# Performance work log

Hardware: AMD Instinct MI355X
Metric: run time of the kernel (lower is better)

The kernel has to match this reference:

```python
import jax, jax.numpy as jnp
import numpy as np

B, NA, NE = 1024, 15, 16
N_AGENTS = NA + 1
BN = B * N_AGENTS
D_OWN = D_ALL = D_EN = 32
H, NH, NMOVE, RD = 256, 4, 6, 8
HD = H // NH
GATE = 1.0
NEG = -1e9  # stand-in for -inf (safe under autodiff)


def _gelu(x):
    return jax.nn.gelu(x, approximate=False)  # torch nn.GELU default is exact


def _ln(x, g, b, eps=1e-5):
    m = x.mean(-1, keepdims=True)
    v = ((x - m) ** 2).mean(-1, keepdims=True)
    return (x - m) * jax.lax.rsqrt(v + eps) * g + b


def _masked_mean(x, mask, axis):
    w = mask[..., None].astype(x.dtype)
    return (x * w).sum(axis) / jnp.clip(w.sum(axis), 1e-8)


def _mha(q, kv, mask, Wq, Wk, Wv, Wo):
    # q: [BN,H], kv: [BN,M,H], mask: [BN,M] bool
    bn = q.shape[0]
    qh = (q @ Wq.T).reshape(bn, NH, HD)
    kh = (kv @ Wk.T).reshape(bn, -1, NH, HD)
    vh = (kv @ Wv.T).reshape(bn, -1, NH, HD)
    scores = jnp.einsum('bhd,bmhd->bhm', qh, kh) / np.sqrt(HD)
    scores = jnp.where(mask[:, None, :], scores, NEG)
    attn = jax.nn.softmax(scores, axis=-1)
    ctx = jnp.einsum('bhm,bmhd->bhd', attn, vh).reshape(bn, H)
    return ctx @ Wo.T


def setup_inputs() -> dict:
    key = jax.random.key(0)
    ks = iter(jax.random.split(key, 64))
    nrm = lambda *s: jax.random.normal(next(ks), s, dtype=jnp.float32)
    w = lambda o, i: nrm(o, i) * 0.02
    inp = dict(
        bs=B,
        own_feats=nrm(BN, 1, D_OWN),
        ally_feats=nrm(BN, NA, D_ALL),
        enemy_feats=nrm(BN, NE, D_EN),
        hidden_state=nrm(B, N_AGENTS, H),
        own_W=w(H, D_OWN), own_b=jnp.zeros(H),
        ally_W=w(H, D_ALL), ally_b=jnp.zeros(H),
        en_W=w(H, D_EN), en_b=jnp.zeros(H),
        aA_Wq=w(H, H), aA_Wk=w(H, H), aA_Wv=w(H, H), aA_Wo=w(H, H),
        aE_Wq=w(H, H), aE_Wk=w(H, H), aE_Wv=w(H, H), aE_Wo=w(H, H),
        fuse_W1=w(H, 3 * H), fuse_b1=jnp.zeros(H), fuse_g1=jnp.ones(H), fuse_be1=jnp.zeros(H),
        fuse_W2=w(H, H), fuse_b2=jnp.zeros(H),
        pool_W1=w(128, 3 * H), pool_b1=jnp.zeros(128), pool_g1=jnp.ones(128), pool_be1=jnp.zeros(128),
        pool_W2=w(128, 128), pool_b2=jnp.zeros(128),
        role_W1=w(128, 128), role_b1=jnp.zeros(128), role_g1=jnp.ones(128), role_be1=jnp.zeros(128),
        role_W2=w(RD, 128), role_b2=jnp.zeros(RD),
        rln_g=jnp.ones(RD), rln_b=jnp.zeros(RD),
        gru_Wih=w(3 * H, H + RD), gru_Whh=w(3 * H, H),
        gru_bih=jnp.zeros(3 * H), gru_bhh=jnp.zeros(3 * H),
        qn_W=w(NMOVE, H), qn_b=jnp.zeros(NMOVE),
        qp_W=w(H, H + RD), kp_W=w(H, H),
    )
    return inp


def reference(bs, own_feats, ally_feats, enemy_feats, hidden_state,
              own_W, own_b, ally_W, ally_b, en_W, en_b,
              aA_Wq, aA_Wk, aA_Wv, aA_Wo, aE_Wq, aE_Wk, aE_Wv, aE_Wo,
              fuse_W1, fuse_b1, fuse_g1, fuse_be1, fuse_W2, fuse_b2,
              pool_W1, pool_b1, pool_g1, pool_be1, pool_W2, pool_b2,
              role_W1, role_b1, role_g1, role_be1, role_W2, role_b2,
              rln_g, rln_b, gru_Wih, gru_Whh, gru_bih, gru_bhh,
              qn_W, qn_b, qp_W, kp_W):
    ally_mask = ~jnp.all(ally_feats == 0, axis=-1)   # [BN,Na]
    enemy_mask = ~jnp.all(enemy_feats == 0, axis=-1)  # [BN,Ne]

    own_e = own_feats @ own_W.T + own_b        # [BN,1,H]
    ally_e = ally_feats @ ally_W.T + ally_b    # [BN,Na,H]
    enemy_e = enemy_feats @ en_W.T + en_b      # [BN,Ne,H]
    self_emb = own_e[:, 0]                     # [BN,H]

    cA = _mha(self_emb, ally_e, ally_mask, aA_Wq, aA_Wk, aA_Wv, aA_Wo)
    cE = _mha(self_emb, enemy_e, enemy_mask, aE_Wq, aE_Wk, aE_Wv, aE_Wo)

    # fuse MLP: Linear -> GELU -> LN -> Linear
    f_in = jnp.concatenate([self_emb, cA, cE], axis=-1)
    h0 = _ln(_gelu(f_in @ fuse_W1.T + fuse_b1), fuse_g1, fuse_be1) @ fuse_W2.T + fuse_b2

    pA = _masked_mean(ally_e, ally_mask, 1)
    pE = _masked_mean(enemy_e, enemy_mask, 1)
    p_in = jnp.concatenate([self_emb, pA, pE], axis=-1)
    pooled = _ln(_gelu(p_in @ pool_W1.T + pool_b1), pool_g1, pool_be1) @ pool_W2.T + pool_b2
    r = jnp.tanh(_ln(_gelu(pooled @ role_W1.T + role_b1), role_g1, role_be1) @ role_W2.T + role_b2)
    r = _ln(r, rln_g, rln_b)

    # GRUCell (torch convention)
    h_prev = hidden_state.reshape(-1, H)
    x = jnp.concatenate([h0, GATE * r], axis=-1)
    gi = x @ gru_Wih.T + gru_bih
    gh = h_prev @ gru_Whh.T + gru_bhh
    i_r, i_z, i_n = jnp.split(gi, 3, axis=-1)
    h_r, h_z, h_n = jnp.split(gh, 3, axis=-1)
    rg = jax.nn.sigmoid(i_r + h_r)
    zg = jax.nn.sigmoid(i_z + h_z)
    ng = jnp.tanh(i_n + rg * h_n)
    h_cur = (1.0 - zg) * ng + zg * h_prev

    q_normal = h_cur @ qn_W.T + qn_b  # [BN,n_move]

    q_vec = jnp.concatenate([h_cur, GATE * r], axis=-1) @ qp_W.T  # [BN,H]
    k_vec = enemy_e @ kp_W.T                                       # [BN,Ne,H]
    logits = jnp.einsum('bj,bmj->bm', q_vec, k_vec) / np.sqrt(H)
    logits = jnp.where(enemy_mask, logits, NEG)
    denom = jnp.clip(enemy_mask.sum(-1, keepdims=True), 1).astype(logits.dtype)
    mean_valid = jnp.where(enemy_mask, logits, 0.0).sum(-1, keepdims=True) / denom
    q_interact = logits - mean_valid

    Q = jnp.concatenate([q_normal, q_interact], axis=-1)
    h_out = h_cur.reshape(bs, N_AGENTS, H)
    return Q, h_out
```

## Files before the change

### kernel.cpp

```cpp
#include <hip/hip_runtime.h>
#include <hip/hip_bf16.h>


#define MROWS 16384

typedef __attribute__((ext_vector_type(8))) short short8;
typedef __attribute__((ext_vector_type(4))) float float4v;

__device__ __forceinline__ unsigned short f2b(float f) {
    __hip_bfloat16 h = __float2bfloat16(f);
    return *reinterpret_cast<unsigned short*>(&h);
}
__device__ __forceinline__ float b2f(unsigned short u) {
    __hip_bfloat16 h;
    *reinterpret_cast<unsigned short*>(&h) = u;
    return __bfloat162float(h);
}
__device__ __forceinline__ void gll16(const unsigned short* g, unsigned short* l) {
    __builtin_amdgcn_global_load_lds((const __attribute__((address_space(1))) void*)g,
                                     (__attribute__((address_space(3))) void*)l, 16, 0, 0);
}

__global__ void cvt_misc(const float* __restrict__ hidden, const float* __restrict__ ownf,
                         unsigned short* __restrict__ XG, unsigned short* __restrict__ OWNb,
// ... 1 lines not shown
    int idx = blockIdx.x * 256 + threadIdx.x;
    const int nh = MROWS * 64;
    const int no = MROWS * 8;
    if (idx < nh) {
        int row = idx >> 6, c4 = (idx & 63) * 4;
        float4 v = *(const float4*)(hidden + (size_t)row * 256 + c4);
        unsigned short* d = XG + (size_t)row * 520 + 264 + c4;
        d[0] = f2b(v.x); d[1] = f2b(v.y); d[2] = f2b(v.z); d[3] = f2b(v.w);
    } else if (idx < nh + no) {
        int j = idx - nh;
        int row = j >> 3, c4 = (j & 7) * 4;
        float4 v = *(const float4*)(ownf + (size_t)row * 32 + c4);
        unsigned short* d = OWNb + (size_t)row * 32 + c4;
        d[0] = f2b(v.x); d[1] = f2b(v.y); d[2] = f2b(v.z); d[3] = f2b(v.w);
    } else if (idx < nh + no + 16) {
        int j = idx - nh - no;
        ((uint4*)zbuf)[j] = make_uint4(0u, 0u, 0u, 0u);
    }
}

struct TOp {
    int type;
    const float* A; int sAi, sAk;
    const float* B; int sBj, sBk;
    void* O; int sOi;
    int I, J, K;
    int nb; int aB, bB, oB;
};
struct TOpSet { int n; int tiles[26]; TOp ops[26]; };

__global__ __launch_bounds__(256)
void compose_tiled(TOpSet S) {
    int t = blockIdx.x;
    int op = 0;
    while (op < S.n && t >= S.tiles[op]) { t -= S.tiles[op]; op++; }
    if (op >= S.n) return;
    TOp o = S.ops[op];
    int ti = (o.I + 31) >> 5, tj = (o.J + 31) >> 5;
    int per = ti * tj;
    int b = t / per;
    int rem = t - b * per;
    int i0 = (rem / tj) * 32, j0 = (rem % tj) * 32;
    int tid = threadIdx.x;
    if (o.type >= 2) {
        for (int e = tid; e < 1024; e += 256) {
            int r = e >> 5, c = e & 31;
            int i = i0 + r, j = j0 + c;
            if (i < o.I && j < o.J) {
                unsigned short v = 0;
                if (o.type == 2) v = f2b(o.A[(long)b * o.aB + (long)i * o.sAi + (long)j * o.sAk]);
                ((unsigned short*)o.O)[(long)b * o.oB + (long)i * o.sOi + j] = v;
            }
        }
        return;
    }
    __shared__ float As[32][33];
    __shared__ float Bs[32][33];
    int tx = tid & 15, ty = tid >> 4;
    float a00 = 0.f, a01 = 0.f, a10 = 0.f, a11 = 0.f;
    const float* Ab = o.A + (long)b * o.aB;
    const float* Bb = o.B + (long)b * o.bB;
    for (int k0 = 0; k0 < o.K; k0 += 32) {
        for (int e = tid; e < 1024; e += 256) {
            int r = e >> 5, c = e & 31;
            As[r][c] = (i0 + r < o.I && k0 + c < o.K)
                       ? Ab[(long)(i0 + r) * o.sAi + (long)(k0 + c) * o.sAk] : 0.f;
// ... 5 lines not shown
        for (int k = 0; k < 32; k++) {
            float x0 = As[ty * 2][k], x1 = As[ty * 2 + 1][k];
            float y0 = Bs[k][tx * 2], y1 = Bs[k][tx * 2 + 1];
            a00 += x0 * y0; a01 += x0 * y1; a10 += x1 * y0; a11 += x1 * y1;
        }
        __syncthreads();
    }
    int i = i0 + ty * 2, j = j0 + tx * 2;
    float vals[2][2] = {{a00, a01}, {a10, a11}};
#pragma unroll
    for (int di = 0; di < 2; di++)
#pragma unroll
        for (int dj = 0; dj < 2; dj++) {
            int ii = i + di, jj = j + dj;
            if (ii < o.I && jj < o.J) {
                long oidx = (long)b * o.oB + (long)ii * o.sOi + jj;
                if (o.type == 0) ((unsigned short*)o.O)[oidx] = f2b(vals[di][dj]);
                else ((float*)o.O)[oidx] = vals[di][dj];
            }
        }
}

struct MOp { const float* A; int sAi; const float* x; const float* b1; const float* b2; float* out; int I, K; };
struct MOpSet { int n; int waves[10]; MOp ops[10]; };

__global__ void mv_ops(MOpSet S) {
    int wid = blockIdx.x * 4 + (threadIdx.x >> 6);
    int lane = threadIdx.x & 63;
    int op = 0;
    while (op < S.n && wid >= S.waves[op]) { wid -= S.waves[op]; op++; }
    if (op >= S.n) return;
    MOp o = S.ops[op];
    float s = 0.f;
    for (int k = lane; k < o.K; k += 64) s += o.A[(long)wid * o.sAi + k] * o.x[k];
    for (int off = 32; off; off >>= 1) s += __shfl_xor(s, off, 64);
    if (lane == 0) {
        if (o.b1) s += o.b1[wid];
        if (o.b2) s += o.b2[wid];
        o.out[wid] = s;
    }
}

__global__ __launch_bounds__(256, 4)
void gemm_bf16(const unsigned short* __restrict__ A, int lda,
               const unsigned short* __restrict__ W,
               const float* __restrict__ bias,
               unsigned short* __restrict__ C, int ldc,
               int N, int K, int act,
               const unsigned short* __restrict__ zbuf) {
    __shared__ __align__(16) unsigned short As[128 * 32];
    __shared__ __align__(16) unsigned short Bs[128 * 32];
    int tid = threadIdx.x;
    int m0 = blockIdx.x * 128, n0 = blockIdx.y * 128;
    int wave = tid >> 6, lane = tid & 63;
    int wm = (wave & 1) * 64, wn = (wave >> 1) * 64;
    int l16 = lane & 15, quad = lane >> 4;

    float4v acc[4][4];
#pragma unroll
    for (int i = 0; i < 4; i++)
#pragma unroll
        for (int j = 0; j < 4; j++) acc[i][j] = (float4v){0.f, 0.f, 0.f, 0.f};

    int s0 = tid, s1 = tid + 256;
    int row0 = s0 >> 2, seg0 = (s0 & 3) * 8;
    int row1 = s1 >> 2, seg1 = (s1 & 3) * 8;
    const unsigned short* Arow0 = A + (size_t)(m0 + row0) * lda;
    const unsigned short* Arow1 = A + (size_t)(m0 + row1) * lda;
    const unsigned short* Wrow0 = (n0 + row0 < N) ? W + (size_t)(n0 + row0) * K : nullptr;
    const unsigned short* Wrow1 = (n0 + row1 < N) ? W + (size_t)(n0 + row1) * K : nullptr;
    unsigned short* ldsA0 = As + (size_t)(wave * 64) * 8;
    unsigned short* ldsA1 = As + (size_t)(wave * 64 + 256) * 8;
    unsigned short* ldsB0 = Bs + (size_t)(wave * 64) * 8;
    unsigned short* ldsB1 = Bs + (size_t)(wave * 64 + 256) * 8;

    for (int k0 = 0; k0 < K; k0 += 32) {
        int ka0 = k0 + seg0, ka1 = k0 + seg1;
        gll16((ka0 < K) ? Arow0 + ka0 : zbuf, ldsA0);
        gll16((ka1 < K) ? Arow1 + ka1 : zbuf, ldsA1);
        gll16((ka0 < K && Wrow0) ? Wrow0 + ka0 : zbuf, ldsB0);
        gll16((ka1 < K && Wrow1) ? Wrow1 + ka1 : zbuf, ldsB1);
        __syncthreads();
        short8 a[4], b[4];
#pragma unroll
        for (int i = 0; i < 4; i++) {
            a[i] = *(const short8*)(&As[(wm + i * 16 + l16) * 32 + quad * 8]);
            b[i] = *(const short8*)(&Bs[(wn + i * 16 + l16) * 32 + quad * 8]);
        }
#pragma unroll
        for (int i = 0; i < 4; i++)
#pragma unroll
            for (int j = 0; j < 4; j++)
                acc[i][j] = __builtin_amdgcn_mfma_f32_16x16x32_bf16(a[i], b[j], acc[i][j], 0, 0, 0);
        __syncthreads();
    }
#pragma unroll
    for (int i = 0; i < 4; i++) {
#pragma unroll
        for (int j = 0; j < 4; j++) {
#pragma unroll
            for (int rr = 0; rr < 4; rr++) {
                int rowm = m0 + wm + i * 16 + quad * 4 + rr;
                int coln = wn + j * 16 + l16;
                if (n0 + coln >= N) continue;
                float v = acc[i][j][rr];
                if (bias) v += bias[n0 + coln];
                if (act == 1) v = 0.5f * v * (1.f + erff(v * 0.70710678f));
                C[(size_t)rowm * ldc + n0 + coln] = f2b(v);
            }
        }
    }
}

__global__ void ln_fp(const unsigned short* __restrict__ FPC,
                      const float* __restrict__ g1, const float* __restrict__ be1,
                      const float* __restrict__ g2, const float* __restrict__ be2,
                      unsigned short* __restrict__ XG, unsigned short* __restrict__ T2) {
    int row = blockIdx.x, t = threadIdx.x;
    float v = b2f(FPC[(size_t)row * 384 + t]);
// ... 7 lines not shown
        float ts = rs[0] + rs[1] + rs[2] + rs[3], tq = rq[0] + rq[1] + rq[2] + rq[3];
        float mean = ts * (1.f / 256.f);
        float var = tq * (1.f / 256.f) - mean * mean;
        float o = (v - mean) * rsqrtf(var + 1e-5f) * g1[t] + be1[t];
        XG[(size_t)row * 520 + t] = f2b(o);
    } else {
        int tt = t - 256;
        float ts = rs[4] + rs[5], tq = rq[4] + rq[5];
        float mean = ts * (1.f / 128.f);
        float var = tq * (1.f / 128.f) - mean * mean;
        float o = (v - mean) * rsqrtf(var + 1e-5f) * g2[tt] + be2[tt];
        T2[(size_t)row * 128 + tt] = f2b(o);
    }
}

__global__ __launch_bounds__(256)
void glue_attn(const float* __restrict__ allyf, const float* __restrict__ enemyf,
               const float* __restrict__ ownf, const unsigned short* __restrict__ QKS,
               unsigned short* __restrict__ X) {
    __shared__ float af[4][495];
    __shared__ float ef[4][528];
    __shared__ float qk[4][256];
    __shared__ float attnA[4][64];
    __shared__ float attnE[4][64];
    __shared__ float mskA[4][16];
    __shared__ float mskE[4][16];
    int tid = threadIdx.x;
    size_t rb = (size_t)blockIdx.x * 4;

    for (int idx = tid; idx < 1920; idx += 256) {
        int r = idx / 480, w0 = idx % 480;
        af[r][(w0 >> 5) * 33 + (w0 & 31)] = allyf[(rb + r) * 480 + w0];
    }
    for (int idx = tid; idx < 2048; idx += 256) {
        int r = idx >> 9, w0 = idx & 511;
        ef[r][(w0 >> 5) * 33 + (w0 & 31)] = enemyf[(rb + r) * 512 + w0];
    }
    for (int idx = tid; idx < 1024; idx += 256)
        qk[idx >> 8][idx & 255] = b2f(QKS[(rb + (idx >> 8)) * 256 + (idx & 255)]);
    if (tid < 128) {
        int r = tid >> 5, c = tid & 31;
        X[(rb + r) * 360 + c] = f2b(ownf[(rb + r) * 32 + c]);
    } else if (tid < 152) {
        int r = (tid - 128) / 6, c = 98 + (tid - 128) % 6;
        X[(rb + r) * 360 + c] = 0;
    }
    __syncthreads();

    {
        int r = tid >> 6, lane = tid & 63;
        if (lane < 15) {
            bool nz = false;
            for (int d = 0; d < 32; d++) nz |= (af[r][lane * 33 + d] != 0.f);
            mskA[r][lane] = nz ? 1.f : 0.f;
        } else if (lane == 15) {
            mskA[r][15] = 0.f;
        } else if (lane < 32) {
            int mm = lane - 16;
            bool nz = false;
            for (int d = 0; d < 32; d++) nz |= (ef[r][mm * 33 + d] != 0.f);
            mskE[r][mm] = nz ? 1.f : 0.f;
        }
    }
    __syncthreads();

    int r = tid >> 6, lane = tid & 63;
    int h = lane >> 4, m = lane & 15;
    {
        float sc = -3.0e38f;
        if (m < 15) {
            float s = 0.f;
            for (int d = 0; d < 32; d++) s += qk[r][h * 32 + d] * af[r][m * 33 + d];
            sc = (mskA[r][m] > 0.f) ? s * 0.125f : -1e9f;
        }
        float mx = sc;
        for (int o = 8; o; o >>= 1) mx = fmaxf(mx, __shfl_xor(mx, o, 64));
        float e = (m < 15) ? __expf(sc - mx) : 0.f;
        float sm = e;
        for (int o = 8; o; o >>= 1) sm += __shfl_xor(sm, o, 64);
        attnA[r][h * 16 + m] = e / sm;
    }
// ... 62 lines not shown
    float acc = b2[t];
    const float* w = W2 + t * 128;
    for (int d = 0; d < 128; d++)
        acc += w[d] * ((t3[r][d] - mean) * rstd * gl[d] + bl[d]);
    float v = tanhf(acc);
    float mn = v;
    for (int o = 4; o; o >>= 1) mn += __shfl_xor(mn, o, 8);
    mn *= 0.125f;
    float dv = v - mn, qq = dv * dv;
    for (int o = 4; o; o >>= 1) qq += __shfl_xor(qq, o, 8);
    qq *= 0.125f;
    size_t row = (size_t)blockIdx.x * 32 + r;
    XG[row * 520 + 256 + t] = f2b(dv * rsqrtf(qq + 1e-5f) * rg[t] + rb[t]);
}

__global__ void glue_gru(const unsigned short* __restrict__ G, const float* __restrict__ hp,
                         float* __restrict__ hout, unsigned short* __restrict__ XQ,
                         const unsigned short* __restrict__ XG) {
    size_t row = blockIdx.x;
    int i = threadIdx.x;
    size_t b = row * 1024;
    float rg = 1.f / (1.f + __expf(-b2f(G[b + i])));
    float zg = 1.f / (1.f + __expf(-b2f(G[b + 256 + i])));
    float ng = tanhf(b2f(G[b + 512 + i]) + rg * b2f(G[b + 768 + i]));
    float h = (1.f - zg) * ng + zg * hp[row * 256 + i];
    hout[row * 256 + i] = h;
    XQ[row * 264 + i] = f2b(h);
    if (i < 8) XQ[row * 264 + 256 + i] = XG[row * 520 + 256 + i];
}

__global__ __launch_bounds__(256)
void glue_final(const unsigned short* __restrict__ QWS, const float* __restrict__ efeats,
                const float* __restrict__ qnb, float* __restrict__ Q) {
    __shared__ float ef[8][528];
    __shared__ float qw[8][40];
    int tid = threadIdx.x;
    size_t rb = (size_t)blockIdx.x * 8;
    for (int idx = tid; idx < 4096; idx += 256) {
        int r = idx >> 9, w0 = idx & 511;
        ef[r][(w0 >> 5) * 33 + (w0 & 31)] = efeats[(rb + r) * 512 + w0];
    }
    for (int idx = tid; idx < 320; idx += 256) {
        int r = idx / 40, c = idx % 40;
        qw[r][c] = b2f(QWS[(rb + r) * 40 + c]);
    }
    __syncthreads();
    int r = tid >> 5, t = tid & 31;
    size_t row = rb + r;
    float lg = 0.f, mk = 0.f;
    if (t < 16) {
        const float* fr = ef[r] + t * 33;
        bool nz = false;
        float s = 0.f;
        for (int d = 0; d < 32; d++) { nz |= (fr[d] != 0.f); s += qw[r][d] * fr[d]; }
        mk = nz ? 1.f : 0.f;
        lg = (s + qw[r][32]) * 0.0625f;
    }
    float sv = mk * lg, cv = mk;
    for (int o = 8; o; o >>= 1) { sv += __shfl_xor(sv, o, 64); cv += __shfl_xor(cv, o, 64); }
    float mean = sv / fmaxf(cv, 1.f);
    if (t < 16) Q[row * 22 + 6 + t] = (mk > 0.f ? lg : -1e9f) - mean;
    if (t < 6) Q[row * 22 + t] = qw[r][33 + t] + qnb[t];
}

extern "C" void kernel_launch(void* const* d_in, const int* in_sizes, int n_in,
                              void* d_out, int out_size, void* d_ws, size_t ws_size,
                              hipStream_t stream) {
    const float* own_feats = (const float*)d_in[1];
    const float* ally_feats = (const float*)d_in[2];
    const float* enemy_feats = (const float*)d_in[3];
    const float* hidden = (const float*)d_in[4];
    const float* own_W = (const float*)d_in[5];   const float* own_b = (const float*)d_in[6];
    const float* ally_W = (const float*)d_in[7];  const float* ally_b = (const float*)d_in[8];
    const float* en_W = (const float*)d_in[9];    const float* en_b = (const float*)d_in[10];
    const float* aA_Wq = (const float*)d_in[11];  const float* aA_Wk = (const float*)d_in[12];
    const float* aA_Wv = (const float*)d_in[13];  const float* aA_Wo = (const float*)d_in[14];
    const float* aE_Wq = (const float*)d_in[15];  const float* aE_Wk = (const float*)d_in[16];
// ... 9 lines not shown
    const float* role_W2 = (const float*)d_in[35]; const float* role_b2 = (const float*)d_in[36];
    const float* rln_g = (const float*)d_in[37];   const float* rln_b = (const float*)d_in[38];
    const float* gru_Wih = (const float*)d_in[39]; const float* gru_Whh = (const float*)d_in[40];
    const float* gru_bih = (const float*)d_in[41]; const float* gru_bhh = (const float*)d_in[42];
    const float* qn_W = (const float*)d_in[43];    const float* qn_b = (const float*)d_in[44];
    const float* qp_W = (const float*)d_in[45];    const float* kp_W = (const float*)d_in[46];

    char* wsp = (char*)d_ws;
    size_t off = 0;
    auto alloc = [&](size_t bytes) { void* p = wsp + off; off = (off + bytes + 255) & ~(size_t)255; return p; };

    unsigned short* X    = (unsigned short*)alloc((size_t)MROWS * 360 * 2);
    unsigned short* XG   = (unsigned short*)alloc((size_t)MROWS * 520 * 2);
    unsigned short* FPC  = (unsigned short*)alloc((size_t)MROWS * 384 * 2);
    unsigned short* GIb  = (unsigned short*)alloc((size_t)MROWS * 1024 * 2);
    unsigned short* XQ   = (unsigned short*)alloc((size_t)MROWS * 264 * 2);
    unsigned short* T2b  = (unsigned short*)alloc((size_t)MROWS * 128 * 2);
    unsigned short* T3b  = (unsigned short*)alloc((size_t)MROWS * 128 * 2);
    unsigned short* QKSb = (unsigned short*)alloc((size_t)MROWS * 256 * 2);
    unsigned short* QWSb = (unsigned short*)alloc((size_t)MROWS * 40 * 2);
    unsigned short* OWNb = (unsigned short*)alloc((size_t)MROWS * 32 * 2);
    unsigned short* FPW  = (unsigned short*)alloc(384 * 360 * 2);
    unsigned short* WGRU = (unsigned short*)alloc(1024 * 520 * 2);
    unsigned short* QWSW = (unsigned short*)alloc(40 * 264 * 2);
    unsigned short* WQKSO= (unsigned short*)alloc(256 * 32 * 2);
    unsigned short* rpW  = (unsigned short*)alloc(128 * 128 * 2);
    unsigned short* zbuf = (unsigned short*)alloc(256);
    float* WkAp = (float*)alloc(256 * 32 * 4);
    float* WvAp = (float*)alloc(256 * 32 * 4);
    float* WkEp = (float*)alloc(256 * 32 * 4);
    float* WvEp = (float*)alloc(256 * 32 * 4);
    float* Wkpp = (float*)alloc(256 * 32 * 4);
    float* WQKS_AE = (float*)alloc(256 * 256 * 4);
    float* WoVA = (float*)alloc(256 * 128 * 4);
    float* WoVE = (float*)alloc(256 * 128 * 4);
    float* bvAp = (float*)alloc(256 * 4);
    float* bvEp = (float*)alloc(256 * 4);
    float* bkpp = (float*)alloc(256 * 4);
    float* vall = (float*)alloc(768 * 4);
    float* qksb = (float*)alloc(256 * 4);
    float* fpb  = (float*)alloc(384 * 4);
    float* gbias= (float*)alloc(1024 * 4);
    float* rpb  = (float*)alloc(128 * 4);

    float* Qout = (float*)d_out;
    float* Hout = Qout + (size_t)MROWS * 22;

    auto tilesOf = [](const TOp& o) {
        return o.nb * (((o.I + 31) / 32) * ((o.J + 31) / 32));
    };

    cvt_misc<<<(MROWS * 64 + MROWS * 8 + 16 + 255) / 256, 256, 0, stream>>>(hidden, own_feats, XG, OWNb, zbuf);

    {
        MOpSet S; S.n = 5; int waves = 0;
        S.ops[0] = {aA_Wv, 256, ally_b, nullptr, nullptr, bvAp, 256, 256};
        S.ops[1] = {aE_Wv, 256, en_b, nullptr, nullptr, bvEp, 256, 256};
        S.ops[2] = {kp_W, 256, en_b, nullptr, nullptr, bkpp, 256, 256};
        S.ops[3] = {nullptr, 0, nullptr, own_b, nullptr, vall, 256, 0};
        S.ops[4] = {role_W1, 128, pool_b2, role_b1, nullptr, rpb, 128, 128};
        for (int i = 0; i < S.n; i++) { S.waves[i] = S.ops[i].I; waves += S.ops[i].I; }
        mv_ops<<<(waves + 3) / 4, 256, 0, stream>>>(S);
    }
    {
        TOpSet S; S.n = 0; int grid = 0;
        auto add = [&](TOp o) { S.tiles[S.n] = tilesOf(o); grid += S.tiles[S.n]; S.ops[S.n++] = o; };
        add({1, aA_Wk, 256, 1, ally_W, 1, 32, WkAp, 32, 256, 32, 256, 1, 0, 0, 0});
        add({1, aA_Wv, 256, 1, ally_W, 1, 32, WvAp, 32, 256, 32, 256, 1, 0, 0, 0});
        add({1, aE_Wk, 256, 1, en_W, 1, 32, WkEp, 32, 256, 32, 256, 1, 0, 0, 0});
        add({1, aE_Wv, 256, 1, en_W, 1, 32, WvEp, 32, 256, 32, 256, 1, 0, 0, 0});
        add({1, kp_W, 256, 1, en_W, 1, 32, Wkpp, 32, 256, 32, 256, 1, 0, 0, 0});
        compose_tiled<<<grid, 256, 0, stream>>>(S);
    }
    {
        TOpSet S; S.n = 0; int grid = 0;
        auto add = [&](TOp o) { S.tiles[S.n] = tilesOf(o); grid += S.tiles[S.n]; S.ops[S.n++] = o; };
        add({1, WkAp, 1, 32, aA_Wq, 1, 256, WQKS_AE, 256, 32, 256, 64, 4, 2048, 16384, 8192});
        add({1, WkEp, 1, 32, aE_Wq, 1, 256, WQKS_AE + 128 * 256, 256, 32, 256, 64, 4, 2048, 16384, 8192});
        add({1, aA_Wo, 256, 1, WvAp, 1, 32, WoVA, 128, 256, 32, 64, 4, 64, 2048, 32});
        add({1, aE_Wo, 256, 1, WvEp, 1, 32, WoVE, 128, 256, 32, 64, 4, 64, 2048, 32});
        compose_tiled<<<grid, 256, 0, stream>>>(S);
    }
    {
        MOpSet S; S.n = 3; int waves = 0;
        S.ops[0] = {aA_Wo, 256, bvAp, nullptr, nullptr, vall + 256, 256, 256};
        S.ops[1] = {aE_Wo, 256, bvEp, nullptr, nullptr, vall + 512, 256, 256};
        S.ops[2] = {WQKS_AE, 256, own_b, nullptr, nullptr, qksb, 256, 256};
        for (int i = 0; i < S.n; i++) { S.waves[i] = S.ops[i].I; waves += S.ops[i].I; }
        mv_ops<<<(waves + 3) / 4, 256, 0, stream>>>(S);
    }
    {
        MOpSet S; S.n = 5; int waves = 0;
        S.ops[0] = {fuse_W1, 768, vall, fuse_b1, nullptr, fpb, 256, 768};
        S.ops[1] = {pool_W1, 768, vall, pool_b1, nullptr, fpb + 256, 128, 256};
        S.ops[2] = {gru_Wih, 264, fuse_b2, gru_bih, gru_bhh, gbias, 512, 256};
        S.ops[3] = {gru_Wih + 512 * 264, 264, fuse_b2, gru_bih + 512, nullptr, gbias + 512, 256, 256};
        S.ops[4] = {nullptr, 0, nullptr, gru_bhh + 512, nullptr, gbias + 768, 256, 0};
        for (int i = 0; i < S.n; i++) { S.waves[i] = S.ops[i].I; waves += S.ops[i].I; }
        mv_ops<<<(waves + 3) / 4, 256, 0, stream>>>(S);
    }
    {
        TOpSet S; S.n = 0; int grid = 0;
        auto add = [&](TOp o) { S.tiles[S.n] = tilesOf(o); grid += S.tiles[S.n]; S.ops[S.n++] = o; };
        add({0, fuse_W1, 768, 1, own_W, 1, 32, FPW, 360, 256, 32, 256, 1, 0, 0, 0});
        add({3, nullptr, 0, 0, nullptr, 0, 0, FPW + 32, 360, 256, 72, 0, 1, 0, 0, 0});
        add({0, fuse_W1 + 256, 768, 1, WoVA, 1, 128, FPW + 104, 360, 256, 128, 256, 1, 0, 0, 0});
        add({0, fuse_W1 + 512, 768, 1, WoVE, 1, 128, FPW + 232, 360, 256, 128, 256, 1, 0, 0, 0});
        add({0, pool_W1, 768, 1, own_W, 1, 32, FPW + 256 * 360, 360, 128, 32, 256, 1, 0, 0, 0});
        add({0, pool_W1 + 256, 768, 1, ally_W, 1, 32, FPW + 256 * 360 + 32, 360, 128, 32, 256, 1, 0, 0, 0});
        add({0, pool_W1 + 512, 768, 1, en_W, 1, 32, FPW + 256 * 360 + 64, 360, 128, 32, 256, 1, 0, 0, 0});
        add({0, pool_W1 + 256, 768, 1, ally_b, 0, 1, FPW + 256 * 360 + 96, 360, 128, 1, 256, 1, 0, 0, 0});
        add({0, pool_W1 + 512, 768, 1, en_b, 0, 1, FPW + 256 * 360 + 97, 360, 128, 1, 256, 1, 0, 0, 0});
        add({3, nullptr, 0, 0, nullptr, 0, 0, FPW + 256 * 360 + 98, 360, 128, 262, 0, 1, 0, 0, 0});
        add({0, gru_Wih, 264, 1, fuse_W2, 1, 256, WGRU, 520, 512, 256, 256, 1, 0, 0, 0});
        add({2, gru_Wih + 256, 264, 1, nullptr, 0, 0, WGRU + 256, 520, 512, 8, 0, 1, 0, 0, 0});
        add({2, gru_Whh, 256, 1, nullptr, 0, 0, WGRU + 264, 520, 512, 256, 0, 1, 0, 0, 0});
        add({0, gru_Wih + 512 * 264, 264, 1, fuse_W2, 1, 256, WGRU + 512 * 520, 520, 256, 256, 256, 1, 0, 0, 0});
        add({2, gru_Wih + 512 * 264 + 256, 264, 1, nullptr, 0, 0, WGRU + 512 * 520 + 256, 520, 256, 8, 0, 1, 0, 0, 0});
        add({3, nullptr, 0, 0, nullptr, 0, 0, WGRU + 512 * 520 + 264, 520, 256, 256, 0, 1, 0, 0, 0});
        add({3, nullptr, 0, 0, nullptr, 0, 0, WGRU + 768 * 520, 520, 256, 264, 0, 1, 0, 0, 0});
        add({2, gru_Whh + 512 * 256, 256, 1, nullptr, 0, 0, WGRU + 768 * 520 + 264, 520, 256, 256, 0, 1, 0, 0, 0});
        add({0, Wkpp, 1, 32, qp_W, 1, 264, QWSW, 264, 32, 264, 256, 1, 0, 0, 0});
        add({0, bkpp, 0, 1, qp_W, 1, 264, QWSW + 32 * 264, 264, 1, 264, 256, 1, 0, 0, 0});
        add({2, qn_W, 256, 1, nullptr, 0, 0, QWSW + 33 * 264, 264, 6, 256, 0, 1, 0, 0, 0});
        add({3, nullptr, 0, 0, nullptr, 0, 0, QWSW + 33 * 264 + 256, 264, 6, 8, 0, 1, 0, 0, 0});
        add({3, nullptr, 0, 0, nullptr, 0, 0, QWSW + 39 * 264, 264, 1, 264, 0, 1, 0, 0, 0});
        add({0, WQKS_AE, 256, 1, own_W, 1, 32, WQKSO, 32, 256, 32, 256, 1, 0, 0, 0});
        add({0, role_W1, 128, 1, pool_W2, 1, 128, rpW, 128, 128, 128, 128, 1, 0, 0, 0});
        compose_tiled<<<grid, 256, 0, stream>>>(S);
    }

    auto gemm = [&](const unsigned short* A, int lda, const unsigned short* Wm, const float* bias,
                    unsigned short* C, int ldc, int N, int K, int act) {
        gemm_bf16<<<dim3(MROWS / 128, (N + 127) / 128), 256, 0, stream>>>(A, lda, Wm, bias, C, ldc, N, K, act, zbuf);
    };

    gemm(OWNb, 32, WQKSO, qksb, QKSb, 256, 256, 32, 0);
    glue_attn<<<MROWS / 4, 256, 0, stream>>>(ally_feats, enemy_feats, own_feats, QKSb, X);
    gemm(X, 360, FPW, fpb, FPC, 384, 384, 360, 1);
    ln_fp<<<MROWS, 384, 0, stream>>>(FPC, fuse_g1, fuse_be1, pool_g1, pool_be1, XG, T2b);
    gemm(T2b, 128, rpW, rpb, T3b, 128, 128, 128, 1);
    ln_role<<<MROWS / 32, 256, 0, stream>>>(T3b, role_g1, role_be1, role_W2, role_b2, rln_g, rln_b, XG);
    gemm(XG, 520, WGRU, gbias, GIb, 1024, 1024, 520, 0);
    glue_gru<<<MROWS, 256, 0, stream>>>(GIb, hidden, Hout, XQ, XG);
    gemm(XQ, 264, QWSW, nullptr, QWSb, 40, 40, 264, 0);
    glue_final<<<MROWS / 8, 256, 0, stream>>>(QWSb, enemy_feats, qn_b, Qout);
}
```

Baseline: 485.9 us.

## Split GRU GEMM to skip zero blocks, fuse GRU tail with Q head, merge prep launches

```diff
diff --git a/kernel.cpp b/kernel.cpp
--- a/kernel.cpp
+++ b/kernel.cpp
@@ -39,8 +39,7 @@
         unsigned short* d = OWNb + (size_t)row * 32 + c4;
         d[0] = f2b(v.x); d[1] = f2b(v.y); d[2] = f2b(v.z); d[3] = f2b(v.w);
     } else if (idx < nh + no + 16) {
-        int j = idx - nh - no;
-        ((uint4*)zbuf)[j] = make_uint4(0u, 0u, 0u, 0u);
+        ((uint4*)zbuf)[idx - nh - no] = make_uint4(0u, 0u, 0u, 0u);
     }
 }
 
@@ -51,6 +50,7 @@
     void* O; int sOi;
     int I, J, K;
     int nb; int aB, bB, oB;
+    const float* bias1; const float* bias2;
 };
 struct TOpSet { int n; int tiles[26]; TOp ops[26]; };
 
@@ -72,9 +72,13 @@
             int r = e >> 5, c = e & 31;
             int i = i0 + r, j = j0 + c;
             if (i < o.I && j < o.J) {
-                unsigned short v = 0;
-                if (o.type == 2) v = f2b(o.A[(long)b * o.aB + (long)i * o.sAi + (long)j * o.sAk]);
-                ((unsigned short*)o.O)[(long)b * o.oB + (long)i * o.sOi + j] = v;
+                long oidx = (long)b * o.oB + (long)i * o.sOi + j;
+                if (o.type == 3) { ((unsigned short*)o.O)[oidx] = 0; }
+                else {
+                    float v = o.A[(long)b * o.aB + (long)i * o.sAi + (long)j * o.sAk];
+                    if (o.type == 2) ((unsigned short*)o.O)[oidx] = f2b(v);
+                    else ((float*)o.O)[oidx] = v;
+                }
             }
         }
         return;
@@ -110,31 +114,14 @@
         for (int dj = 0; dj < 2; dj++) {
             int ii = i + di, jj = j + dj;
             if (ii < o.I && jj < o.J) {
+                float v = vals[di][dj];
+                if (o.bias1) v += o.bias1[ii];
+                if (o.bias2) v += o.bias2[ii];
                 long oidx = (long)b * o.oB + (long)ii * o.sOi + jj;
-                if (o.type == 0) ((unsigned short*)o.O)[oidx] = f2b(vals[di][dj]);
-                else ((float*)o.O)[oidx] = vals[di][dj];
+                if (o.type == 0) ((unsigned short*)o.O)[oidx] = f2b(v);
+                else ((float*)o.O)[oidx] = v;
             }
         }
-}
-
-struct MOp { const float* A; int sAi; const float* x; const float* b1; const float* b2; float* out; int I, K; };
-struct MOpSet { int n; int waves[10]; MOp ops[10]; };
-
-__global__ void mv_ops(MOpSet S) {
-    int wid = blockIdx.x * 4 + (threadIdx.x >> 6);
-    int lane = threadIdx.x & 63;
-    int op = 0;
-    while (op < S.n && wid >= S.waves[op]) { wid -= S.waves[op]; op++; }
-    if (op >= S.n) return;
-    MOp o = S.ops[op];
-    float s = 0.f;
-    for (int k = lane; k < o.K; k += 64) s += o.A[(long)wid * o.sAi + k] * o.x[k];
-    for (int off = 32; off; off >>= 1) s += __shfl_xor(s, off, 64);
-    if (lane == 0) {
-        if (o.b1) s += o.b1[wid];
-        if (o.b2) s += o.b2[wid];
-        o.out[wid] = s;
-    }
 }
 
 __global__ __launch_bounds__(256, 4)
@@ -147,7 +134,7 @@
     __shared__ __align__(16) unsigned short As[128 * 32];
     __shared__ __align__(16) unsigned short Bs[128 * 32];
     int tid = threadIdx.x;
-    int m0 = blockIdx.x * 128, n0 = blockIdx.y * 128;
+    int n0 = blockIdx.x * 128, m0 = blockIdx.y * 128;
     int wave = tid >> 6, lane = tid & 63;
     int wm = (wave & 1) * 64, wn = (wave >> 1) * 64;
     int l16 = lane & 15, quad = lane >> 4;
@@ -163,8 +150,8 @@
     int row1 = s1 >> 2, seg1 = (s1 & 3) * 8;
     const unsigned short* Arow0 = A + (size_t)(m0 + row0) * lda;
     const unsigned short* Arow1 = A + (size_t)(m0 + row1) * lda;
-    const unsigned short* Wrow0 = (n0 + row0 < N) ? W + (size_t)(n0 + row0) * K : nullptr;
-    const unsigned short* Wrow1 = (n0 + row1 < N) ? W + (size_t)(n0 + row1) * K : nullptr;
+    const unsigned short* Wrow0 = W + (size_t)(n0 + row0) * K;
+    const unsigned short* Wrow1 = W + (size_t)(n0 + row1) * K;
     unsigned short* ldsA0 = As + (size_t)(wave * 64) * 8;
     unsigned short* ldsA1 = As + (size_t)(wave * 64 + 256) * 8;
     unsigned short* ldsB0 = Bs + (size_t)(wave * 64) * 8;
@@ -174,8 +161,8 @@
         int ka0 = k0 + seg0, ka1 = k0 + seg1;
         gll16((ka0 < K) ? Arow0 + ka0 : zbuf, ldsA0);
         gll16((ka1 < K) ? Arow1 + ka1 : zbuf, ldsA1);
-        gll16((ka0 < K && Wrow0) ? Wrow0 + ka0 : zbuf, ldsB0);
-        gll16((ka1 < K && Wrow1) ? Wrow1 + ka1 : zbuf, ldsB1);
+        gll16((ka0 < K) ? Wrow0 + ka0 : zbuf, ldsB0);
+        gll16((ka1 < K) ? Wrow1 + ka1 : zbuf, ldsB1);
         __syncthreads();
         short8 a[4], b[4];
 #pragma unroll
@@ -198,7 +185,6 @@
             for (int rr = 0; rr < 4; rr++) {
                 int rowm = m0 + wm + i * 16 + quad * 4 + rr;
                 int coln = wn + j * 16 + l16;
-                if (n0 + coln >= N) continue;
                 float v = acc[i][j][rr];
                 if (bias) v += bias[n0 + coln];
                 if (act == 1) v = 0.5f * v * (1.f + erff(v * 0.70710678f));
@@ -236,57 +222,58 @@
     }
 }
 
-__global__ __launch_bounds__(256)
+__global__ __launch_bounds__(128)
 void glue_attn(const float* __restrict__ allyf, const float* __restrict__ enemyf,
                const float* __restrict__ ownf, const unsigned short* __restrict__ QKS,
                unsigned short* __restrict__ X) {
-    __shared__ float af[4][495];
-    __shared__ float ef[4][528];
-    __shared__ float qk[4][256];
-    __shared__ float attnA[4][64];
-    __shared__ float attnE[4][64];
-    __shared__ float mskA[4][16];
-    __shared__ float mskE[4][16];
+    __shared__ float af[2][495];
+    __shared__ float ef[2][528];
+    __shared__ float qk[2][256];
+    __shared__ float attnA[2][64];
+    __shared__ float attnE[2][64];
+    __shared__ float mskA[2][16];
+    __shared__ float mskE[2][16];
     int tid = threadIdx.x;
-    size_t rb = (size_t)blockIdx.x * 4;
-
-    for (int idx = tid; idx < 1920; idx += 256) {
-        int r = idx / 480, w0 = idx % 480;
-        af[r][(w0 >> 5) * 33 + (w0 & 31)] = allyf[(rb + r) * 480 + w0];
-    }
-    for (int idx = tid; idx < 2048; idx += 256) {
-        int r = idx >> 9, w0 = idx & 511;
-        ef[r][(w0 >> 5) * 33 + (w0 & 31)] = enemyf[(rb + r) * 512 + w0];
-    }
-    for (int idx = tid; idx < 1024; idx += 256)
+    size_t rb = (size_t)blockIdx.x * 2;
+
+    for (int idx = tid; idx < 240; idx += 128) {
+        int r = idx / 120, w0 = (idx % 120) * 4;
+        float4 v = *(const float4*)(allyf + (rb + r) * 480 + w0);
+        float* d = &af[r][(w0 >> 5) * 33 + (w0 & 31)];
+        d[0] = v.x; d[1] = v.y; d[2] = v.z; d[3] = v.w;
+    }
+    for (int idx = tid; idx < 256; idx += 128) {
+        int r = idx >> 7, w0 = (idx & 127) * 4;
+        float4 v = *(const float4*)(enemyf + (rb + r) * 512 + w0);
+        float* d = &ef[r][(w0 >> 5) * 33 + (w0 & 31)];
+        d[0] = v.x; d[1] = v.y; d[2] = v.z; d[3] = v.w;
+    }
+    for (int idx = tid; idx < 512; idx += 128)
         qk[idx >> 8][idx & 255] = b2f(QKS[(rb + (idx >> 8)) * 256 + (idx & 255)]);
-    if (tid < 128) {
+    if (tid < 64) {
         int r = tid >> 5, c = tid & 31;
         X[(rb + r) * 360 + c] = f2b(ownf[(rb + r) * 32 + c]);
-    } else if (tid < 152) {
-        int r = (tid - 128) / 6, c = 98 + (tid - 128) % 6;
+    } else if (tid < 76) {
+        int j = tid - 64, r = j / 6, c = 98 + j % 6;
         X[(rb + r) * 360 + c] = 0;
     }
     __syncthreads();
 
-    {
-        int r = tid >> 6, lane = tid & 63;
-        if (lane < 15) {
-            bool nz = false;
-            for (int d = 0; d < 32; d++) nz |= (af[r][lane * 33 + d] != 0.f);
-            mskA[r][lane] = nz ? 1.f : 0.f;
-        } else if (lane == 15) {
-            mskA[r][15] = 0.f;
-        } else if (lane < 32) {
-            int mm = lane - 16;
-            bool nz = false;
-            for (int d = 0; d < 32; d++) nz |= (ef[r][mm * 33 + d] != 0.f);
-            mskE[r][mm] = nz ? 1.f : 0.f;
-        }
-    }
-    __syncthreads();
-
     int r = tid >> 6, lane = tid & 63;
+    if (lane < 15) {
+        bool nz = false;
+        for (int d = 0; d < 32; d++) nz |= (af[r][lane * 33 + d] != 0.f);
+        mskA[r][lane] = nz ? 1.f : 0.f;
+    } else if (lane == 15) {
+        mskA[r][15] = 0.f;
+    } else if (lane < 32) {
+        int mm = lane - 16;
+        bool nz = false;
+        for (int d = 0; d < 32; d++) nz |= (ef[r][mm * 33 + d] != 0.f);
+        mskE[r][mm] = nz ? 1.f : 0.f;
+    }
+    __syncthreads();
+
     int h = lane >> 4, m = lane & 15;
     {
         float sc = -3.0e38f;
@@ -379,53 +366,55 @@
     XG[row * 520 + 256 + t] = f2b(dv * rsqrtf(qq + 1e-5f) * rg[t] + rb[t]);
 }
 
-__global__ void glue_gru(const unsigned short* __restrict__ G, const float* __restrict__ hp,
-                         float* __restrict__ hout, unsigned short* __restrict__ XQ,
-                         const unsigned short* __restrict__ XG) {
+__global__ __launch_bounds__(320)
+void glue_tail(const unsigned short* __restrict__ G, const float* __restrict__ hp,
+               const unsigned short* __restrict__ XG, const unsigned short* __restrict__ QWSW,
+               const float* __restrict__ enemyf, const float* __restrict__ qnb,
+               float* __restrict__ Q, float* __restrict__ Hout) {
+    __shared__ float xq[264];
+    __shared__ float efs[528];
+    __shared__ float qws[40];
     size_t row = blockIdx.x;
-    int i = threadIdx.x;
-    size_t b = row * 1024;
-    float rg = 1.f / (1.f + __expf(-b2f(G[b + i])));
-    float zg = 1.f / (1.f + __expf(-b2f(G[b + 256 + i])));
-    float ng = tanhf(b2f(G[b + 512 + i]) + rg * b2f(G[b + 768 + i]));
-    float h = (1.f - zg) * ng + zg * hp[row * 256 + i];
-    hout[row * 256 + i] = h;
-    XQ[row * 264 + i] = f2b(h);
-    if (i < 8) XQ[row * 264 + 256 + i] = XG[row * 520 + 256 + i];
-}
-
-__global__ __launch_bounds__(256)
-void glue_final(const unsigned short* __restrict__ QWS, const float* __restrict__ efeats,
-                const float* __restrict__ qnb, float* __restrict__ Q) {
-    __shared__ float ef[8][528];
-    __shared__ float qw[8][40];
-    int tid = threadIdx.x;
-    size_t rb = (size_t)blockIdx.x * 8;
-    for (int idx = tid; idx < 4096; idx += 256) {
-        int r = idx >> 9, w0 = idx & 511;
-        ef[r][(w0 >> 5) * 33 + (w0 & 31)] = efeats[(rb + r) * 512 + w0];
-    }
-    for (int idx = tid; idx < 320; idx += 256) {
-        int r = idx / 40, c = idx % 40;
-        qw[r][c] = b2f(QWS[(rb + r) * 40 + c]);
-    }
-    __syncthreads();
-    int r = tid >> 5, t = tid & 31;
-    size_t row = rb + r;
-    float lg = 0.f, mk = 0.f;
+    int t = threadIdx.x;
+    for (int idx = t; idx < 512; idx += 320)
+        efs[(idx >> 5) * 33 + (idx & 31)] = enemyf[row * 512 + idx];
+    if (t < 256) {
+        size_t b = row * 1024;
+        float rg = 1.f / (1.f + __expf(-b2f(G[b + t])));
+        float zg = 1.f / (1.f + __expf(-b2f(G[b + 256 + t])));
+        float ng = tanhf(b2f(G[b + 512 + t]) + rg * b2f(G[b + 768 + t]));
+        float h = (1.f - zg) * ng + zg * hp[row * 256 + t];
+        Hout[row * 256 + t] = h;
+        xq[t] = h;
+    } else if (t < 264) {
+        xq[t] = b2f(XG[row * 520 + t]);
+    }
+    __syncthreads();
+    {
+        int o = t >> 3, sub = t & 7;
+        const unsigned short* wr = QWSW + o * 264 + sub * 33;
+        const float* xv = xq + sub * 33;
+        float s = 0.f;
+        for (int i = 0; i < 33; i++) s += b2f(wr[i]) * xv[i];
+        for (int off = 4; off; off >>= 1) s += __shfl_xor(s, off, 8);
+        if (sub == 0) qws[o] = s;
+    }
+    __syncthreads();
     if (t < 16) {
-        const float* fr = ef[r] + t * 33;
+        const float* fr = efs + t * 33;
         bool nz = false;
         float s = 0.f;
-        for (int d = 0; d < 32; d++) { nz |= (fr[d] != 0.f); s += qw[r][d] * fr[d]; }
-        mk = nz ? 1.f : 0.f;
-        lg = (s + qw[r][32]) * 0.0625f;
-    }
-    float sv = mk * lg, cv = mk;
-    for (int o = 8; o; o >>= 1) { sv += __shfl_xor(sv, o, 64); cv += __shfl_xor(cv, o, 64); }
-    float mean = sv / fmaxf(cv, 1.f);
-    if (t < 16) Q[row * 22 + 6 + t] = (mk > 0.f ? lg : -1e9f) - mean;
-    if (t < 6) Q[row * 22 + t] = qw[r][33 + t] + qnb[t];
+        for (int d = 0; d < 32; d++) { nz |= (fr[d] != 0.f); s += qws[d] * fr[d]; }
+        float mk = nz ? 1.f : 0.f;
+        float lg = (s + qws[32]) * 0.0625f;
+        float sv = mk * lg, cv = mk;
+        for (int o = 8; o; o >>= 1) { sv += __shfl_xor(sv, o, 16); cv += __shfl_xor(cv, o, 16); }
+        float mean = sv / fmaxf(cv, 1.f);
+        Q[row * 22 + 6 + t] = (mk > 0.f ? lg : -1e9f) - mean;
+    } else if (t >= 64 && t < 70) {
+        int j = t - 64;
+        Q[row * 22 + j] = qws[33 + j] + qnb[j];
+    }
 }
 
 extern "C" void kernel_launch(void* const* d_in, const int* in_sizes, int n_in,
@@ -465,14 +454,14 @@
     unsigned short* XG   = (unsigned short*)alloc((size_t)MROWS * 520 * 2);
     unsigned short* FPC  = (unsigned short*)alloc((size_t)MROWS * 384 * 2);
     unsigned short* GIb  = (unsigned short*)alloc((size_t)MROWS * 1024 * 2);
-    unsigned short* XQ   = (unsigned short*)alloc((size_t)MROWS * 264 * 2);
     unsigned short* T2b  = (unsigned short*)alloc((size_t)MROWS * 128 * 2);
     unsigned short* T3b  = (unsigned short*)alloc((size_t)MROWS * 128 * 2);
     unsigned short* QKSb = (unsigned short*)alloc((size_t)MROWS * 256 * 2);
-    unsigned short* QWSb = (unsigned short*)alloc((size_t)MROWS * 40 * 2);
     unsigned short* OWNb = (unsigned short*)alloc((size_t)MROWS * 32 * 2);
     unsigned short* FPW  = (unsigned short*)alloc(384 * 360 * 2);
-    unsigned short* WGRU = (unsigned short*)alloc(1024 * 520 * 2);
+    unsigned short* WRZ  = (unsigned short*)alloc(512 * 520 * 2);
+    unsigned short* WIN  = (unsigned short*)alloc(256 * 264 * 2);
+    unsigned short* WHN  = (unsigned short*)alloc(256 * 256 * 2);
     unsigned short* QWSW = (unsigned short*)alloc(40 * 264 * 2);
     unsigned short* WQKSO= (unsigned short*)alloc(256 * 32 * 2);
     unsigned short* rpW  = (unsigned short*)alloc(128 * 128 * 2);
@@ -497,6 +486,13 @@
     float* Qout = (float*)d_out;
     float* Hout = Qout + (size_t)MROWS * 22;
 
+    auto mk = [](int type, const float* A, int sAi, int sAk, const float* B, int sBj, int sBk,
+                 void* O, int sOi, int I, int J, int K, int nb = 1, int aB = 0, int bB = 0,
+                 int oB = 0, const float* b1 = nullptr, const float* b2 = nullptr) {
+        TOp o; o.type = type; o.A = A; o.sAi = sAi; o.sAk = sAk; o.B = B; o.sBj = sBj;
+        o.sBk = sBk; o.O = O; o.sOi = sOi; o.I = I; o.J = J; o.K = K; o.nb = nb;
+        o.aB = aB; o.bB = bB; o.oB = oB; o.bias1 = b1; o.bias2 = b2; return o;
+    };
     auto tilesOf = [](const TOp& o) {
         return o.nb * (((o.I + 31) / 32) * ((o.J + 31) / 32));
     };
@@ -504,96 +500,79 @@
     cvt_misc<<<(MROWS * 64 + MROWS * 8 + 16 + 255) / 256, 256, 0, stream>>>(hidden, own_feats, XG, OWNb, zbuf);
 
     {
-        MOpSet S; S.n = 5; int waves = 0;
-        S.ops[0] = {aA_Wv, 256, ally_b, nullptr, nullptr, bvAp, 256, 256};
-        S.ops[1] = {aE_Wv, 256, en_b, nullptr, nullptr, bvEp, 256, 256};
-        S.ops[2] = {kp_W, 256, en_b, nullptr, nullptr, bkpp, 256, 256};
-        S.ops[3] = {nullptr, 0, nullptr, own_b, nullptr, vall, 256, 0};
-        S.ops[4] = {role_W1, 128, pool_b2, role_b1, nullptr, rpb, 128, 128};
-        for (int i = 0; i < S.n; i++) { S.waves[i] = S.ops[i].I; waves += S.ops[i].I; }
-        mv_ops<<<(waves + 3) / 4, 256, 0, stream>>>(S);
+        TOpSet S; S.n = 0; int grid = 0;
+        auto add = [&](TOp o) { S.tiles[S.n] = tilesOf(o); grid += S.tiles[S.n]; S.ops[S.n++] = o; };
+        add(mk(1, aA_Wk, 256, 1, ally_W, 1, 32, WkAp, 32, 256, 32, 256));
+        add(mk(1, aA_Wv, 256, 1, ally_W, 1, 32, WvAp, 32, 256, 32, 256));
+        add(mk(1, aE_Wk, 256, 1, en_W, 1, 32, WkEp, 32, 256, 32, 256));
+        add(mk(1, aE_Wv, 256, 1, en_W, 1, 32, WvEp, 32, 256, 32, 256));
+        add(mk(1, kp_W, 256, 1, en_W, 1, 32, Wkpp, 32, 256, 32, 256));
+        add(mk(1, aA_Wv, 256, 1, ally_b, 0, 1, bvAp, 1, 256, 1, 256));
+        add(mk(1, aE_Wv, 256, 1, en_b, 0, 1, bvEp, 1, 256, 1, 256));
+        add(mk(1, kp_W, 256, 1, en_b, 0, 1, bkpp, 1, 256, 1, 256));
+        add(mk(4, own_b, 1, 1, nullptr, 0, 0, vall, 1, 256, 1, 0));
+        add(mk(1, role_W1, 128, 1, pool_b2, 0, 1, rpb, 1, 128, 1, 128, 1, 0, 0, 0, role_b1));
+        add(mk(1, gru_Wih, 264, 1, fuse_b2, 0, 1, gbias, 1, 512, 1, 256, 1, 0, 0, 0, gru_bih, gru_bhh));
+        add(mk(1, gru_Wih + 512 * 264, 264, 1, fuse_b2, 0, 1, gbias + 512, 1, 256, 1, 256, 1, 0, 0, 0, gru_bih + 512));
+        add(mk(4, gru_bhh + 512, 1, 1, nullptr, 0, 0, gbias + 768, 1, 256, 1, 0));
+        compose_tiled<<<grid, 256, 0, stream>>>(S);
     }
     {
         TOpSet S; S.n = 0; int grid = 0;
         auto add = [&](TOp o) { S.tiles[S.n] = tilesOf(o); grid += S.tiles[S.n]; S.ops[S.n++] = o; };
-        add({1, aA_Wk, 256, 1, ally_W, 1, 32, WkAp, 32, 256, 32, 256, 1, 0, 0, 0});
-        add({1, aA_Wv, 256, 1, ally_W, 1, 32, WvAp, 32, 256, 32, 256, 1, 0, 0, 0});
-        add({1, aE_Wk, 256, 1, en_W, 1, 32, WkEp, 32, 256, 32, 256, 1, 0, 0, 0});
-        add({1, aE_Wv, 256, 1, en_W, 1, 32, WvEp, 32, 256, 32, 256, 1, 0, 0, 0});
-        add({1, kp_W, 256, 1, en_W, 1, 32, Wkpp, 32, 256, 32, 256, 1, 0, 0, 0});
+        add(mk(1, WkAp, 1, 32, aA_Wq, 1, 256, WQKS_AE, 256, 32, 256, 64, 4, 2048, 16384, 8192));
+        add(mk(1, WkEp, 1, 32, aE_Wq, 1, 256, WQKS_AE + 128 * 256, 256, 32, 256, 64, 4, 2048, 16384, 8192));
+        add(mk(1, aA_Wo, 256, 1, WvAp, 1, 32, WoVA, 128, 256, 32, 64, 4, 64, 2048, 32));
+        add(mk(1, aE_Wo, 256, 1, WvEp, 1, 32, WoVE, 128, 256, 32, 64, 4, 64, 2048, 32));
+        add(mk(1, aA_Wo, 256, 1, bvAp, 0, 1, vall + 256, 1, 256, 1, 256));
+        add(mk(1, aE_Wo, 256, 1, bvEp, 0, 1, vall + 512, 1, 256, 1, 256));
         compose_tiled<<<grid, 256, 0, stream>>>(S);
     }
     {
         TOpSet S; S.n = 0; int grid = 0;
         auto add = [&](TOp o) { S.tiles[S.n] = tilesOf(o); grid += S.tiles[S.n]; S.ops[S.n++] = o; };
-        add({1, WkAp, 1, 32, aA_Wq, 1, 256, WQKS_AE, 256, 32, 256, 64, 4, 2048, 16384, 8192});
-        add({1, WkEp, 1, 32, aE_Wq, 1, 256, WQKS_AE + 128 * 256, 256, 32, 256, 64, 4, 2048, 16384, 8192});
-        add({1, aA_Wo, 256, 1, WvAp, 1, 32, WoVA, 128, 256, 32, 64, 4, 64, 2048, 32});
-        add({1, aE_Wo, 256, 1, WvEp, 1, 32, WoVE, 128, 256, 32, 64, 4, 64, 2048, 32});
-        compose_tiled<<<grid, 256, 0, stream>>>(S);
-    }
-    {
-        MOpSet S; S.n = 3; int waves = 0;
-        S.ops[0] = {aA_Wo, 256, bvAp, nullptr, nullptr, vall + 256, 256, 256};
-        S.ops[1] = {aE_Wo, 256, bvEp, nullptr, nullptr, vall + 512, 256, 256};
-        S.ops[2] = {WQKS_AE, 256, own_b, nullptr, nullptr, qksb, 256, 256};
-        for (int i = 0; i < S.n; i++) { S.waves[i] = S.ops[i].I; waves += S.ops[i].I; }
-        mv_ops<<<(waves + 3) / 4, 256, 0, stream>>>(S);
-    }
-    {
-        MOpSet S; S.n = 5; int waves = 0;
-        S.ops[0] = {fuse_W1, 768, vall, fuse_b1, nullptr, fpb, 256, 768};
-        S.ops[1] = {pool_W1, 768, vall, pool_b1, nullptr, fpb + 256, 128, 256};
-        S.ops[2] = {gru_Wih, 264, fuse_b2, gru_bih, gru_bhh, gbias, 512, 256};
-        S.ops[3] = {gru_Wih + 512 * 264, 264, fuse_b2, gru_bih + 512, nullptr, gbias + 512, 256, 256};
-        S.ops[4] = {nullptr, 0, nullptr, gru_bhh + 512, nullptr, gbias + 768, 256, 0};
-        for (int i = 0; i < S.n; i++) { S.waves[i] = S.ops[i].I; waves += S.ops[i].I; }
-        mv_ops<<<(waves + 3) / 4, 256, 0, stream>>>(S);
-    }
-    {
-        TOpSet S; S.n = 0; int grid = 0;
-        auto add = [&](TOp o) { S.tiles[S.n] = tilesOf(o); grid += S.tiles[S.n]; S.ops[S.n++] = o; };
-        add({0, fuse_W1, 768, 1, own_W, 1, 32, FPW, 360, 256, 32, 256, 1, 0, 0, 0});
-        add({3, nullptr, 0, 0, nullptr, 0, 0, FPW + 32, 360, 256, 72, 0, 1, 0, 0, 0});
-        add({0, fuse_W1 + 256, 768, 1, WoVA, 1, 128, FPW + 104, 360, 256, 128, 256, 1, 0, 0, 0});
-        add({0, fuse_W1 + 512, 768, 1, WoVE, 1, 128, FPW + 232, 360, 256, 128, 256, 1, 0, 0, 0});
-        add({0, pool_W1, 768, 1, own_W, 1, 32, FPW + 256 * 360, 360, 128, 32, 256, 1, 0, 0, 0});
-        add({0, pool_W1 + 256, 768, 1, ally_W, 1, 32, FPW + 256 * 360 + 32, 360, 128, 32, 256, 1, 0, 0, 0});
-        add({0, pool_W1 + 512, 768, 1, en_W, 1, 32, FPW + 256 * 360 + 64, 360, 128, 32, 256, 1, 0, 0, 0});
-        add({0, pool_W1 + 256, 768, 1, ally_b, 0, 1, FPW + 256 * 360 + 96, 360, 128, 1, 256, 1, 0, 0, 0});
-        add({0, pool_W1 + 512, 768, 1, en_b, 0, 1, FPW + 256 * 360 + 97, 360, 128, 1, 256, 1, 0, 0, 0});
-        add({3, nullptr, 0, 0, nullptr, 0, 0, FPW + 256 * 360 + 98, 360, 128, 262, 0, 1, 0, 0, 0});
-        add({0, gru_Wih, 264, 1, fuse_W2, 1, 256, WGRU, 520, 512, 256, 256, 1, 0, 0, 0});
-        add({2, gru_Wih + 256, 264, 1, nullptr, 0, 0, WGRU + 256, 520, 512, 8, 0, 1, 0, 0, 0});
-        add({2, gru_Whh, 256, 1, nullptr, 0, 0, WGRU + 264, 520, 512, 256, 0, 1, 0, 0, 0});
-        add({0, gru_Wih + 512 * 264, 264, 1, fuse_W2, 1, 256, WGRU + 512 * 520, 520, 256, 256, 256, 1, 0, 0, 0});
-        add({2, gru_Wih + 512 * 264 + 256, 264, 1, nullptr, 0, 0, WGRU + 512 * 520 + 256, 520, 256, 8, 0, 1, 0, 0, 0});
-        add({3, nullptr, 0, 0, nullptr, 0, 0, WGRU + 512 * 520 + 264, 520, 256, 256, 0, 1, 0, 0, 0});
-        add({3, nullptr, 0, 0, nullptr, 0, 0, WGRU + 768 * 520, 520, 256, 264, 0, 1, 0, 0, 0});
-        add({2, gru_Whh + 512 * 256, 256, 1, nullptr, 0, 0, WGRU + 768 * 520 + 264, 520, 256, 256, 0, 1, 0, 0, 0});
-        add({0, Wkpp, 1, 32, qp_W, 1, 264, QWSW, 264, 32, 264, 256, 1, 0, 0, 0});
-        add({0, bkpp, 0, 1, qp_W, 1, 264, QWSW + 32 * 264, 264, 1, 264, 256, 1, 0, 0, 0});
-        add({2, qn_W, 256, 1, nullptr, 0, 0, QWSW + 33 * 264, 264, 6, 256, 0, 1, 0, 0, 0});
-        add({3, nullptr, 0, 0, nullptr, 0, 0, QWSW + 33 * 264 + 256, 264, 6, 8, 0, 1, 0, 0, 0});
-        add({3, nullptr, 0, 0, nullptr, 0, 0, QWSW + 39 * 264, 264, 1, 264, 0, 1, 0, 0, 0});
-        add({0, WQKS_AE, 256, 1, own_W, 1, 32, WQKSO, 32, 256, 32, 256, 1, 0, 0, 0});
-        add({0, role_W1, 128, 1, pool_W2, 1, 128, rpW, 128, 128, 128, 128, 1, 0, 0, 0});
+        add(mk(1, WQKS_AE, 256, 1, own_b, 0, 1, qksb, 1, 256, 1, 256));
+        add(mk(1, fuse_W1, 768, 1, vall, 0, 1, fpb, 1, 256, 1, 768, 1, 0, 0, 0, fuse_b1));
+        add(mk(1, pool_W1, 768, 1, own_b, 0, 1, fpb + 256, 1, 128, 1, 256, 1, 0, 0, 0, pool_b1));
+        add(mk(0, WQKS_AE, 256, 1, own_W, 1, 32, WQKSO, 32, 256, 32, 256));
+        add(mk(0, fuse_W1, 768, 1, own_W, 1, 32, FPW, 360, 256, 32, 256));
+        add(mk(3, nullptr, 0, 0, nullptr, 0, 0, FPW + 32, 360, 256, 72, 0));
+        add(mk(0, fuse_W1 + 256, 768, 1, WoVA, 1, 128, FPW + 104, 360, 256, 128, 256));
+        add(mk(0, fuse_W1 + 512, 768, 1, WoVE, 1, 128, FPW + 232, 360, 256, 128, 256));
+        add(mk(0, pool_W1, 768, 1, own_W, 1, 32, FPW + 256 * 360, 360, 128, 32, 256));
+        add(mk(0, pool_W1 + 256, 768, 1, ally_W, 1, 32, FPW + 256 * 360 + 32, 360, 128, 32, 256));
+        add(mk(0, pool_W1 + 512, 768, 1, en_W, 1, 32, FPW + 256 * 360 + 64, 360, 128, 32, 256));
+        add(mk(0, pool_W1 + 256, 768, 1, ally_b, 0, 1, FPW + 256 * 360 + 96, 360, 128, 1, 256));
+        add(mk(0, pool_W1 + 512, 768, 1, en_b, 0, 1, FPW + 256 * 360 + 97, 360, 128, 1, 256));
+        add(mk(3, nullptr, 0, 0, nullptr, 0, 0, FPW + 256 * 360 + 98, 360, 128, 262, 0));
+        add(mk(0, gru_Wih, 264, 1, fuse_W2, 1, 256, WRZ, 520, 512, 256, 256));
+        add(mk(2, gru_Wih + 256, 264, 1, nullptr, 0, 0, WRZ + 256, 520, 512, 8, 0));
+        add(mk(2, gru_Whh, 256, 1, nullptr, 0, 0, WRZ + 264, 520, 512, 256, 0));
+        add(mk(0, gru_Wih + 512 * 264, 264, 1, fuse_W2, 1, 256, WIN, 264, 256, 256, 256));
+        add(mk(2, gru_Wih + 512 * 264 + 256, 264, 1, nullptr, 0, 0, WIN + 256, 264, 256, 8, 0));
+        add(mk(2, gru_Whh + 512 * 256, 256, 1, nullptr, 0, 0, WHN, 256, 256, 256, 0));
+        add(mk(0, Wkpp, 1, 32, qp_W, 1, 264, QWSW, 264, 32, 264, 256));
+        add(mk(0, bkpp, 0, 1, qp_W, 1, 264, QWSW + 32 * 264, 264, 1, 264, 256));
+        add(mk(2, qn_W, 256, 1, nullptr, 0, 0, QWSW + 33 * 264, 264, 6, 256, 0));
+        add(mk(3, nullptr, 0, 0, nullptr, 0, 0, QWSW + 33 * 264 + 256, 264, 6, 8, 0));
+        add(mk(3, nullptr, 0, 0, nullptr, 0, 0, QWSW + 39 * 264, 264, 1, 264, 0));
+        add(mk(0, role_W1, 128, 1, pool_W2, 1, 128, rpW, 128, 128, 128, 128));
         compose_tiled<<<grid, 256, 0, stream>>>(S);
     }
 
     auto gemm = [&](const unsigned short* A, int lda, const unsigned short* Wm, const float* bias,
                     unsigned short* C, int ldc, int N, int K, int act) {
-        gemm_bf16<<<dim3(MROWS / 128, (N + 127) / 128), 256, 0, stream>>>(A, lda, Wm, bias, C, ldc, N, K, act, zbuf);
+        gemm_bf16<<<dim3(N / 128, MROWS / 128), 256, 0, stream>>>(A, lda, Wm, bias, C, ldc, N, K, act, zbuf);
     };
 
     gemm(OWNb, 32, WQKSO, qksb, QKSb, 256, 256, 32, 0);
-    glue_attn<<<MROWS / 4, 256, 0, stream>>>(ally_feats, enemy_feats, own_feats, QKSb, X);
+    glue_attn<<<MROWS / 2, 128, 0, stream>>>(ally_feats, enemy_feats, own_feats, QKSb, X);
     gemm(X, 360, FPW, fpb, FPC, 384, 384, 360, 1);
     ln_fp<<<MROWS, 384, 0, stream>>>(FPC, fuse_g1, fuse_be1, pool_g1, pool_be1, XG, T2b);
     gemm(T2b, 128, rpW, rpb, T3b, 128, 128, 128, 1);
     ln_role<<<MROWS / 32, 256, 0, stream>>>(T3b, role_g1, role_be1, role_W2, role_b2, rln_g, rln_b, XG);
-    gemm(XG, 520, WGRU, gbias, GIb, 1024, 1024, 520, 0);
-    glue_gru<<<MROWS, 256, 0, stream>>>(GIb, hidden, Hout, XQ, XG);
-    gemm(XQ, 264, QWSW, nullptr, QWSb, 40, 40, 264, 0);
-    glue_final<<<MROWS / 8, 256, 0, stream>>>(QWSb, enemy_feats, qn_b, Qout);
-}
+    gemm(XG, 520, WRZ, gbias, GIb, 1024, 512, 520, 0);
+    gemm(XG, 520, WIN, gbias + 512, GIb + 512, 1024, 256, 264, 0);
+    gemm(XG + 264, 520, WHN, gbias + 768, GIb + 768, 1024, 256, 256, 0);
+    glue_tail<<<MROWS, 320, 0, stream>>>(GIb, hidden, XG, QWSW, enemy_feats, qn_b, Qout, Hout);
+}
```

After: 599.7 us. +23.4%, slower.
